# Optimization experiments

Measured on AMD Instinct MI355X. Metric: run time of the kernel, lower is better.

The kernel has to match this reference:

```python
import jax, jax.numpy as jnp
import numpy as np

B, S, H, A, E = 64, 1024, 1024, 512, 512


def setup_inputs() -> dict:
    key = jax.random.key(0)
    ks = jax.random.split(key, 13)
    sc = 0.02
    return {
        "inputs": jax.random.normal(ks[0], (B, E), jnp.float32),
        "states": jax.random.normal(ks[1], (B, H), jnp.float32),
        "encoded": jax.random.normal(ks[2], (B, S, H), jnp.float32),
        "W_enc": jax.random.normal(ks[3], (H, A), jnp.float32) * sc,
        "b_enc": jax.random.normal(ks[4], (A,), jnp.float32) * sc,
        "W_dec": jax.random.normal(ks[5], (H, A), jnp.float32) * sc,
        "b_dec": jax.random.normal(ks[6], (A,), jnp.float32) * sc,
        "w_out": jax.random.normal(ks[7], (A,), jnp.float32) * sc,
        "b_out": jax.random.normal(ks[8], (1,), jnp.float32) * sc,
        "W_ih": jax.random.normal(ks[9], (E + H, 3 * H), jnp.float32) * sc,
        "b_ih": jax.random.normal(ks[10], (3 * H,), jnp.float32) * sc,
        "W_hh": jax.random.normal(ks[11], (H, 3 * H), jnp.float32) * sc,
        "b_hh": jax.random.normal(ks[12], (3 * H,), jnp.float32) * sc,
    }


def reference(inputs, states, encoded, W_enc, b_enc, W_dec, b_dec, w_out, b_out,
              W_ih, b_ih, W_hh, b_hh):
    # setup_memory: project encoder states once  [B,S,H] @ [H,A] -> [B,S,A]
    enc_proj = jnp.einsum('bsh,ha->bsa', encoded, W_enc) + b_enc
    # Bahdanau additive attention
    dec_proj = states @ W_dec + b_dec                       # [B,A]
    scores = jnp.einsum('bsa,a->bs', jnp.tanh(enc_proj + dec_proj[:, None, :]), w_out) + b_out[0]
    weights = jax.nn.softmax(scores, axis=1)                # [B,S]
    attention = jnp.einsum('bs,bsh->bh', weights, encoded)  # [B,H]
    x = jnp.concatenate([inputs, attention], axis=-1)       # [B,E+H]
    # GRUCell (PyTorch gate order r, z, n)
    gi = x @ W_ih + b_ih                                    # [B,3H]
    gh = states @ W_hh + b_hh                               # [B,3H]
    i_r, i_z, i_n = jnp.split(gi, 3, axis=-1)
    h_r, h_z, h_n = jnp.split(gh, 3, axis=-1)
    r = jax.nn.sigmoid(i_r + h_r)
    z = jax.nn.sigmoid(i_z + h_z)
    n = jnp.tanh(i_n + r * h_n)
    h_new = (1.0 - z) * n + z * states
    return h_new
```

## Files before the change

### kernel.cpp

```cpp
#include <hip/hip_runtime.h>
#include <hip/hip_bf16.h>


typedef __attribute__((ext_vector_type(8))) __bf16 bf16x8;
typedef __attribute__((ext_vector_type(4))) __bf16 bf16x4;
typedef __attribute__((ext_vector_type(4))) float f32x4;

__device__ __forceinline__ float fast_tanh(float x) {
  float xa = fminf(fmaxf(x, -15.f), 15.f);
  float e = __expf(2.f * xa);
  return (e - 1.f) / (e + 1.f);
}

__global__ __launch_bounds__(256) void wenc_t_kernel(const float* __restrict__ W,
                                                     __bf16* __restrict__ Wt) {
  __shared__ float tile[32][33];
  int k0 = blockIdx.x * 32, a0 = blockIdx.y * 32;
  int tid = threadIdx.x;
  int r = tid >> 3, c4 = (tid & 7) * 4;
  f32x4 v = *(const f32x4*)(W + (long)(k0 + r) * 512 + a0 + c4);
  tile[r][c4 + 0] = v.x; tile[r][c4 + 1] = v.y;
  tile[r][c4 + 2] = v.z; tile[r][c4 + 3] = v.w;
  __syncthreads();
  int a = tid >> 3, k4 = (tid & 7) * 4;
  bf16x4 o = { (__bf16)tile[k4 + 0][a], (__bf16)tile[k4 + 1][a],
               (__bf16)tile[k4 + 2][a], (__bf16)tile[k4 + 3][a] };
  *(bf16x4*)(Wt + (long)(a0 + a) * 1024 + k0 + k4) = o;
}

__global__ __launch_bounds__(256) void dec_proj_kernel(
    const float* __restrict__ states, const float* __restrict__ W_dec,
    const float* __restrict__ b_enc, const float* __restrict__ b_dec,
    float* __restrict__ addv) {
  int b = blockIdx.x, tid = threadIdx.x;
  int a = blockIdx.y * 256 + tid;
  __shared__ float sl[1024];
  for (int i = tid; i < 1024; i += 256) sl[i] = states[b * 1024 + i];
  __syncthreads();
  float c0 = 0.f, c1 = 0.f, c2 = 0.f, c3 = 0.f;
#pragma unroll 4
  for (int i = 0; i < 256; ++i) {
    c0 += sl[i]         * W_dec[(i)        * 512 + a];
    c1 += sl[i + 256]   * W_dec[(i + 256)  * 512 + a];
    c2 += sl[i + 512]   * W_dec[(i + 512)  * 512 + a];
    c3 += sl[i + 768]   * W_dec[(i + 768)  * 512 + a];
  }
  addv[b * 512 + a] = c0 + c1 + c2 + c3 + b_enc[a] + b_dec[a];
}

__global__ __launch_bounds__(512) void enc_score_kernel(
    const float* __restrict__ encoded,
    const __bf16* __restrict__ Wt,
    const float* __restrict__ addv,
    const float* __restrict__ w_out,
    float* __restrict__ psc)
{
  __shared__ __attribute__((aligned(16))) char smem[67584];
  char* Abase = smem;
  char* Bbase = smem + 32768;
  float* red = (float*)(smem + 65536);

  const int d = blockIdx.x;
  const int xcd = d & 7;
  const int slot = d >> 3;
  const int bn = slot & 3;
  const int bm = ((slot >> 2) << 3) | xcd;

  const int tid = threadIdx.x;
  const int lane = tid & 63;
  const int wid = tid >> 6;
  const int wrow = wid >> 2;
  const int wcol = wid & 3;
  const int lr = lane & 15;
  const int lkb = lane >> 4;

  const long row0 = (long)bm * 128;
  const int col0 = bn * 128;

  f32x4 ra[4];
  bf16x8 rb[2];

  auto loadT = [&](int kt) {
#pragma unroll
    for (int i = 0; i < 4; ++i) {
      int g = i * 512 + tid;
      int row = g >> 4, c4 = g & 15;
      ra[i] = *(const f32x4*)(encoded + (row0 + row) * 1024 + kt * 64 + c4 * 4);
    }
#pragma unroll
    for (int i = 0; i < 2; ++i) {
      int g = i * 512 + tid;
      int col = g >> 3, k8 = g & 7;
      rb[i] = *(const bf16x8*)(Wt + (long)(col0 + col) * 1024 + kt * 64 + k8 * 8);
    }
  };
  auto writeT = [&](int buf) {
#pragma unroll
    for (int i = 0; i < 4; ++i) {
      int g = i * 512 + tid;
      int row = g >> 4, c4 = g & 15;
      bf16x4 v = { (__bf16)ra[i].x, (__bf16)ra[i].y, (__bf16)ra[i].z, (__bf16)ra[i].w };
      int off = (c4 * 8) ^ ((row & 7) << 4);
      *(bf16x4*)(Abase + buf * 16384 + row * 128 + off) = v;
    }
#pragma unroll
    for (int i = 0; i < 2; ++i) {
      int g = i * 512 + tid;
      int col = g >> 3, k8 = g & 7;
      int off = (k8 * 16) ^ ((col & 7) << 4);
      *(bf16x8*)(Bbase + buf * 16384 + col * 128 + off) = rb[i];
    }
  };

  f32x4 acc[4][2];
#pragma unroll
  for (int m = 0; m < 4; ++m)
#pragma unroll
    for (int n = 0; n < 2; ++n) acc[m][n] = (f32x4){0.f, 0.f, 0.f, 0.f};

  loadT(0);
  writeT(0);
  int buf = 0;
  for (int kt = 0; kt < 16; ++kt) {
    __syncthreads();
    if (kt < 15) loadT(kt + 1);
#pragma unroll
    for (int ks = 0; ks < 2; ++ks) {
      bf16x8 af[4], bfv[2];
#pragma unroll
      for (int m = 0; m < 4; ++m) {
        int row = wrow * 64 + m * 16 + lr;
        int kb = (ks * 64 + lkb * 16) ^ ((row & 7) << 4);
        af[m] = *(const bf16x8*)(Abase + buf * 16384 + row * 128 + kb);
      }
#pragma unroll
      for (int n = 0; n < 2; ++n) {
        int col = wcol * 32 + n * 16 + lr;
        int kb = (ks * 64 + lkb * 16) ^ ((col & 7) << 4);
        bfv[n] = *(const bf16x8*)(Bbase + buf * 16384 + col * 128 + kb);
      }
#pragma unroll
      for (int m = 0; m < 4; ++m)
#pragma unroll
        for (int n = 0; n < 2; ++n)
          acc[m][n] = __builtin_amdgcn_mfma_f32_16x16x32_bf16(af[m], bfv[n], acc[m][n], 0, 0, 0);
    }
    if (kt < 15) writeT(buf ^ 1);
    buf ^= 1;
  }

  const int b = bm >> 3;
  const float* addvb = addv + b * 512;
  float rowsum[4][4];
#pragma unroll
  for (int m = 0; m < 4; ++m)
#pragma unroll
    for (int reg = 0; reg < 4; ++reg) rowsum[m][reg] = 0.f;

#pragma unroll
  for (int m = 0; m < 4; ++m) {
#pragma unroll
    for (int n = 0; n < 2; ++n) {
      int col = col0 + wcol * 32 + n * 16 + lr;
      float av = addvb[col];
      float wo = w_out[col];
#pragma unroll
      for (int reg = 0; reg < 4; ++reg)
        rowsum[m][reg] += fast_tanh(acc[m][n][reg] + av) * wo;
    }
  }
#pragma unroll
  for (int m = 0; m < 4; ++m)
#pragma unroll
    for (int reg = 0; reg < 4; ++reg) {
      float v = rowsum[m][reg];
      v += __shfl_xor(v, 1, 64);
      v += __shfl_xor(v, 2, 64);
      v += __shfl_xor(v, 4, 64);
      v += __shfl_xor(v, 8, 64);
      rowsum[m][reg] = v;
    }
  if (lr == 0) {
#pragma unroll
    for (int m = 0; m < 4; ++m)
#pragma unroll
      for (int reg = 0; reg < 4; ++reg)
        red[(wrow * 64 + m * 16 + lkb * 4 + reg) * 4 + wcol] = rowsum[m][reg];
  }
  __syncthreads();
  if (tid < 128)
    psc[(long)bn * 65536 + row0 + tid] =
        red[tid * 4] + red[tid * 4 + 1] + red[tid * 4 + 2] + red[tid * 4 + 3];
}

__global__ __launch_bounds__(256) void softmax_kernel(const float* __restrict__ psc,
                                                      float* __restrict__ wts) {
  int b = blockIdx.x, tid = threadIdx.x;
  __shared__ float sred[8];
  float sc[4];
  float mx = -1e30f;
#pragma unroll
  for (int i = 0; i < 4; ++i) {
    long r = (long)b * 1024 + tid + i * 256;
    sc[i] = psc[r] + psc[65536 + r] + psc[2 * 65536 + r] + psc[3 * 65536 + r];
    mx = fmaxf(mx, sc[i]);
  }
  for (int off = 1; off < 64; off <<= 1) mx = fmaxf(mx, __shfl_xor(mx, off, 64));
  if ((tid & 63) == 0) sred[tid >> 6] = mx;
  __syncthreads();
  mx = fmaxf(fmaxf(sred[0], sred[1]), fmaxf(sred[2], sred[3]));
  float e[4], sum = 0.f;
#pragma unroll
  for (int i = 0; i < 4; ++i) {
    e[i] = __expf(sc[i] - mx);
    sum += e[i];
  }
  for (int off = 1; off < 64; off <<= 1) sum += __shfl_xor(sum, off, 64);
  if ((tid & 63) == 0) sred[4 + (tid >> 6)] = sum;
  __syncthreads();
  sum = sred[4] + sred[5] + sred[6] + sred[7];
  float inv = 1.f / sum;
#pragma unroll
  for (int i = 0; i < 4; ++i) wts[(long)b * 1024 + tid + i * 256] = e[i] * inv;
}

__global__ __launch_bounds__(256) void att_part_kernel(const float* __restrict__ encoded,
                                                       const float* __restrict__ wts,
                                                       float* __restrict__ attp) {
  int chunk = blockIdx.x;
  int b = blockIdx.y;
  int tid = threadIdx.x;
  f32x4 acc0 = (f32x4){0.f, 0.f, 0.f, 0.f};
  f32x4 acc1 = (f32x4){0.f, 0.f, 0.f, 0.f};
  const float* base = encoded + ((long)b * 1024 + chunk * 128) * 1024 + tid * 4;
  const float* w = wts + b * 1024 + chunk * 128;
#pragma unroll 4
  for (int s = 0; s < 128; s += 2) {
    acc0 += *(const f32x4*)(base + (long)s * 1024) * w[s];
    acc1 += *(const f32x4*)(base + (long)(s + 1) * 1024) * w[s + 1];
  }
  *(f32x4*)(attp + ((long)(b * 8 + chunk)) * 1024 + tid * 4) = acc0 + acc1;
}

__global__ __launch_bounds__(256) void xcat_kernel(const float* __restrict__ inputs,
                                                   const float* __restrict__ attp,
                                                   float* __restrict__ xcat) {
  int b = blockIdx.y;
  int k = blockIdx.x * 256 + threadIdx.x;
  float v;
  if (k < 512) {
    v = inputs[b * 512 + k];
  } else {
    int h = k - 512;
    v = 0.f;
#pragma unroll
    for (int c = 0; c < 8; ++c) v += attp[((long)(b * 8 + c)) * 1024 + h];
  }
  xcat[(long)b * 1536 + k] = v;
}

__global__ __launch_bounds__(512) void gru_gemv_kernel(
    const float* __restrict__ xcat, const float* __restrict__ states,
    const float* __restrict__ W_ih, const float* __restrict__ b_ih,
    const float* __restrict__ W_hh, const float* __restrict__ b_hh,
    float* __restrict__ gi, float* __restrict__ gh) {
  __shared__ float sx[12288];
  const int dd = blockIdx.x;
  const int xcd = dd & 7;
  const int n = dd >> 3;
  const int cgrp = xcd + 8 * (n >> 3);
  const int bg = n & 7;
  const int tid = threadIdx.x;
  const int lcol = tid & 255;
  const int bsel = (tid >> 8) * 4;

  if (cgrp < 12) {
    const int col = cgrp * 256 + lcol;
    const float* xb = xcat + (long)bg * 8 * 1536;
    for (int i = tid; i < 3072; i += 512) ((f32x4*)sx)[i] = ((const f32x4*)xb)[i];
    __syncthreads();
    float a0 = b_ih[col], a1 = a0, a2 = a0, a3 = a0;
    const float* x0 = sx + (bsel + 0) * 1536;
    const float* x1 = sx + (bsel + 1) * 1536;
    const float* x2 = sx + (bsel + 2) * 1536;
    const float* x3 = sx + (bsel + 3) * 1536;
    for (int k = 0; k < 1536; k += 4) {
      f32x4 v0 = *(const f32x4*)(x0 + k);
      f32x4 v1 = *(const f32x4*)(x1 + k);
      f32x4 v2 = *(const f32x4*)(x2 + k);
      f32x4 v3 = *(const f32x4*)(x3 + k);
#pragma unroll
      for (int j = 0; j < 4; ++j) {
        float w = W_ih[(long)(k + j) * 3072 + col];
        a0 += v0[j] * w; a1 += v1[j] * w; a2 += v2[j] * w; a3 += v3[j] * w;
      }
    }
    long o = (long)(bg * 8 + bsel) * 3072 + col;
    gi[o] = a0; gi[o + 3072] = a1; gi[o + 6144] = a2; gi[o + 9216] = a3;
  } else {
    const int col = (cgrp - 12) * 256 + lcol;
    const float* sb = states + (long)bg * 8 * 1024;
    for (int i = tid; i < 2048; i += 512) ((f32x4*)sx)[i] = ((const f32x4*)sb)[i];
    __syncthreads();
    float a0 = b_hh[col], a1 = a0, a2 = a0, a3 = a0;
    const float* x0 = sx + (bsel + 0) * 1024;
    const float* x1 = sx + (bsel + 1) * 1024;
    const float* x2 = sx + (bsel + 2) * 1024;
    const float* x3 = sx + (bsel + 3) * 1024;
    for (int k = 0; k < 1024; k += 4) {
      f32x4 v0 = *(const f32x4*)(x0 + k);
      f32x4 v1 = *(const f32x4*)(x1 + k);
      f32x4 v2 = *(const f32x4*)(x2 + k);
      f32x4 v3 = *(const f32x4*)(x3 + k);
#pragma unroll
      for (int j = 0; j < 4; ++j) {
        float w = W_hh[(long)(k + j) * 3072 + col];
        a0 += v0[j] * w; a1 += v1[j] * w; a2 += v2[j] * w; a3 += v3[j] * w;
      }
    }
    long o = (long)(bg * 8 + bsel) * 3072 + col;
    gh[o] = a0; gh[o + 3072] = a1; gh[o + 6144] = a2; gh[o + 9216] = a3;
  }
}

__global__ __launch_bounds__(256) void gate_kernel(const float* __restrict__ gi,
                                                   const float* __restrict__ gh,
                                                   const float* __restrict__ states,
                                                   float* __restrict__ out) {
  int b = blockIdx.y;
  int j = blockIdx.x * 256 + threadIdx.x;
  long o = (long)b * 3072;
  float ir = gi[o + j], hr = gh[o + j];
  float iz = gi[o + 1024 + j], hz = gh[o + 1024 + j];
  float in_ = gi[o + 2048 + j], hn = gh[o + 2048 + j];
  float r = 1.f / (1.f + __expf(-(ir + hr)));
  float z = 1.f / (1.f + __expf(-(iz + hz)));
  float n = fast_tanh(in_ + r * hn);
  out[(long)b * 1024 + j] = (1.f - z) * n + z * states[(long)b * 1024 + j];
}

extern "C" void kernel_launch(void* const* d_in, const int* in_sizes, int n_in,
                              void* d_out, int out_size, void* d_ws, size_t ws_size,
                              hipStream_t stream) {
  const float* inputs  = (const float*)d_in[0];
  const float* states  = (const float*)d_in[1];
  const float* encoded = (const float*)d_in[2];
  const float* W_enc   = (const float*)d_in[3];
  const float* b_enc   = (const float*)d_in[4];
  const float* W_dec   = (const float*)d_in[5];
  const float* b_dec   = (const float*)d_in[6];
  const float* w_out   = (const float*)d_in[7];
  const float* W_ih    = (const float*)d_in[9];
  const float* b_ih    = (const float*)d_in[10];
  const float* W_hh    = (const float*)d_in[11];
  const float* b_hh    = (const float*)d_in[12];
  float* out = (float*)d_out;
  float* ws = (float*)d_ws;

  float* addv = ws;
  float* psc  = ws + 32768;
  float* wts  = ws + 294912;
  float* attp = ws + 360448;
  float* xcat = ws + 884736;
  float* gi   = ws + 983040;
  float* gh   = ws + 1179648;
  __bf16* Wt  = (__bf16*)(ws + 1376256);

  wenc_t_kernel<<<dim3(32, 16), 256, 0, stream>>>(W_enc, Wt);

  dim3 gA(64, 2);
  dec_proj_kernel<<<gA, 256, 0, stream>>>(states, W_dec, b_enc, b_dec, addv);

  enc_score_kernel<<<2048, 512, 0, stream>>>(encoded, Wt, addv, w_out, psc);

  softmax_kernel<<<64, 256, 0, stream>>>(psc, wts);

  dim3 gD(8, 64);
  att_part_kernel<<<gD, 256, 0, stream>>>(encoded, wts, attp);

  dim3 gE(6, 64);
  xcat_kernel<<<gE, 256, 0, stream>>>(inputs, attp, xcat);

  gru_gemv_kernel<<<192, 512, 0, stream>>>(xcat, states, W_ih, b_ih, W_hh, b_hh, gi, gh);

  dim3 gG(4, 64);
  gate_kernel<<<gG, 256, 0, stream>>>(gi, gh, states, out);
}
```

Measured before the change: 324.7 us.

## Restructure enc_score GEMM mainloop with smaller K tiles and deeper register prefetch

The enc_score GEMM mainloop now uses 32-wide K tiles instead of 64, which halves LDS use so more blocks can be resident (launch_bounds minBlocks 4). Two register sets of global loads alternate, so one tile is prefetched while another is computed. The swizzle is reworked to match, and explicit waitcnt, sched_barrier and setprio hints order the LDS reads, MFMAs and barriers by hand. In exchange there are twice as many barriers per K step, and the occupancy target may cap registers and cause spills.

```diff
diff --git a/kernel.cpp b/kernel.cpp
--- a/kernel.cpp
+++ b/kernel.cpp
@@ -48,17 +48,15 @@
   addv[b * 512 + a] = c0 + c1 + c2 + c3 + b_enc[a] + b_dec[a];
 }
 
-__global__ __launch_bounds__(512) void enc_score_kernel(
+__global__ __launch_bounds__(512, 4) void enc_score_kernel(
     const float* __restrict__ encoded,
     const __bf16* __restrict__ Wt,
     const float* __restrict__ addv,
     const float* __restrict__ w_out,
     float* __restrict__ psc)
 {
-  __shared__ __attribute__((aligned(16))) char smem[67584];
-  char* Abase = smem;
-  char* Bbase = smem + 32768;
-  float* red = (float*)(smem + 65536);
+  __shared__ __attribute__((aligned(16))) char smem[34816];
+  float* red = (float*)(smem + 32768);
 
   const int d = blockIdx.x;
   const int xcd = d & 7;
@@ -77,40 +75,16 @@
   const long row0 = (long)bm * 128;
   const int col0 = bn * 128;
 
-  f32x4 ra[4];
-  bf16x8 rb[2];
-
-  auto loadT = [&](int kt) {
-#pragma unroll
-    for (int i = 0; i < 4; ++i) {
-      int g = i * 512 + tid;
-      int row = g >> 4, c4 = g & 15;
-      ra[i] = *(const f32x4*)(encoded + (row0 + row) * 1024 + kt * 64 + c4 * 4);
-    }
-#pragma unroll
-    for (int i = 0; i < 2; ++i) {
-      int g = i * 512 + tid;
-      int col = g >> 3, k8 = g & 7;
-      rb[i] = *(const bf16x8*)(Wt + (long)(col0 + col) * 1024 + kt * 64 + k8 * 8);
-    }
-  };
-  auto writeT = [&](int buf) {
-#pragma unroll
-    for (int i = 0; i < 4; ++i) {
-      int g = i * 512 + tid;
-      int row = g >> 4, c4 = g & 15;
-      bf16x4 v = { (__bf16)ra[i].x, (__bf16)ra[i].y, (__bf16)ra[i].z, (__bf16)ra[i].w };
-      int off = (c4 * 8) ^ ((row & 7) << 4);
-      *(bf16x4*)(Abase + buf * 16384 + row * 128 + off) = v;
-    }
-#pragma unroll
-    for (int i = 0; i < 2; ++i) {
-      int g = i * 512 + tid;
-      int col = g >> 3, k8 = g & 7;
-      int off = (k8 * 16) ^ ((col & 7) << 4);
-      *(bf16x8*)(Bbase + buf * 16384 + col * 128 + off) = rb[i];
-    }
-  };
+  const int srow = tid >> 2;
+  const int sk = tid & 3;
+  const float* aBase = encoded + (row0 + srow) * 1024 + sk * 8;
+  const __bf16* bBase = Wt + (long)(col0 + srow) * 1024 + sk * 8;
+  const int wrOff = srow * 64 + ((sk ^ ((srow >> 1) & 3)) << 4);
+
+  const int aph = ((wrow * 64 + lr) >> 1) & 3;
+  const int aRd = (wrow * 64 + lr) * 64 + ((lkb ^ aph) << 4);
+  const int bph = ((wcol * 32 + lr) >> 1) & 3;
+  const int bRd = (wcol * 32 + lr) * 64 + ((lkb ^ bph) << 4);
 
   f32x4 acc[4][2];
 #pragma unroll
@@ -118,36 +92,66 @@
 #pragma unroll
     for (int n = 0; n < 2; ++n) acc[m][n] = (f32x4){0.f, 0.f, 0.f, 0.f};
 
-  loadT(0);
-  writeT(0);
-  int buf = 0;
-  for (int kt = 0; kt < 16; ++kt) {
-    __syncthreads();
-    if (kt < 15) loadT(kt + 1);
-#pragma unroll
-    for (int ks = 0; ks < 2; ++ks) {
-      bf16x8 af[4], bfv[2];
-#pragma unroll
-      for (int m = 0; m < 4; ++m) {
-        int row = wrow * 64 + m * 16 + lr;
-        int kb = (ks * 64 + lkb * 16) ^ ((row & 7) << 4);
-        af[m] = *(const bf16x8*)(Abase + buf * 16384 + row * 128 + kb);
-      }
-#pragma unroll
-      for (int n = 0; n < 2; ++n) {
-        int col = wcol * 32 + n * 16 + lr;
-        int kb = (ks * 64 + lkb * 16) ^ ((col & 7) << 4);
-        bfv[n] = *(const bf16x8*)(Bbase + buf * 16384 + col * 128 + kb);
-      }
-#pragma unroll
-      for (int m = 0; m < 4; ++m)
-#pragma unroll
-        for (int n = 0; n < 2; ++n)
-          acc[m][n] = __builtin_amdgcn_mfma_f32_16x16x32_bf16(af[m], bfv[n], acc[m][n], 0, 0, 0);
-    }
-    if (kt < 15) writeT(buf ^ 1);
-    buf ^= 1;
-  }
+  f32x4 a0A, a1A; bf16x8 bA;
+  f32x4 a0B, a1B; bf16x8 bB;
+
+#define ISSUE(A0, A1, BV, KT) { \
+    const float* _pa = aBase + (KT) * 32; \
+    A0 = *(const f32x4*)_pa; \
+    A1 = *(const f32x4*)(_pa + 4); \
+    BV = *(const bf16x8*)(bBase + (KT) * 32); }
+
+#define STORE(A0, A1, BV, BUFOFF) { \
+    bf16x8 _wv; \
+    _wv[0] = (__bf16)A0.x; _wv[1] = (__bf16)A0.y; _wv[2] = (__bf16)A0.z; _wv[3] = (__bf16)A0.w; \
+    _wv[4] = (__bf16)A1.x; _wv[5] = (__bf16)A1.y; _wv[6] = (__bf16)A1.z; _wv[7] = (__bf16)A1.w; \
+    *(bf16x8*)(smem + (BUFOFF) + wrOff) = _wv; \
+    *(bf16x8*)(smem + 16384 + (BUFOFF) + wrOff) = BV; }
+
+#define COMPUTE(BUFOFF) { \
+    bf16x8 _af[4], _bf[2]; \
+    _Pragma("unroll") for (int _m = 0; _m < 4; ++_m) \
+      _af[_m] = *(const bf16x8*)(smem + (BUFOFF) + aRd + _m * 1024); \
+    _Pragma("unroll") for (int _n = 0; _n < 2; ++_n) \
+      _bf[_n] = *(const bf16x8*)(smem + 16384 + (BUFOFF) + bRd + _n * 1024); \
+    asm volatile("s_waitcnt lgkmcnt(0)" ::: "memory"); \
+    __builtin_amdgcn_sched_barrier(0); \
+    __builtin_amdgcn_s_setprio(1); \
+    _Pragma("unroll") for (int _m = 0; _m < 4; ++_m) \
+      _Pragma("unroll") for (int _n = 0; _n < 2; ++_n) \
+        acc[_m][_n] = __builtin_amdgcn_mfma_f32_16x16x32_bf16(_af[_m], _bf[_n], acc[_m][_n], 0, 0, 0); \
+    __builtin_amdgcn_s_setprio(0); }
+
+#define BAR() { \
+    asm volatile("s_waitcnt lgkmcnt(0)" ::: "memory"); \
+    __builtin_amdgcn_sched_barrier(0); \
+    __builtin_amdgcn_s_barrier(); \
+    __builtin_amdgcn_sched_barrier(0); }
+
+  ISSUE(a0A, a1A, bA, 0);
+  ISSUE(a0B, a1B, bB, 1);
+  STORE(a0A, a1A, bA, 0);
+  BAR();
+
+  for (int t2 = 0; t2 < 15; ++t2) {
+    ISSUE(a0A, a1A, bA, t2 * 2 + 2);
+    COMPUTE(0);
+    STORE(a0B, a1B, bB, 8192);
+    BAR();
+    ISSUE(a0B, a1B, bB, t2 * 2 + 3);
+    COMPUTE(8192);
+    STORE(a0A, a1A, bA, 0);
+    BAR();
+  }
+  COMPUTE(0);
+  STORE(a0B, a1B, bB, 8192);
+  BAR();
+  COMPUTE(8192);
+
+#undef ISSUE
+#undef STORE
+#undef COMPUTE
+#undef BAR
 
   const int b = bm >> 3;
   const float* addvb = addv + b * 512;
```

New measurement: 328.7 us. Within noise of the previous version (+1.2%).
